# Kernel tuning notes

Measured on AMD Instinct MI355X. Metric: run time of the kernel, lower is better.

Reference implementation:

```python
import jax, jax.numpy as jnp
import numpy as np

SEQ, BATCH, IN_F, STATE, OUT_F = 2048, 32, 256, 512, 256


def setup_inputs() -> dict:
    key = jax.random.key(0)
    k1, k2, k3, k4 = jax.random.split(key, 4)
    x = jax.random.normal(k1, (SEQ, BATCH, IN_F), dtype=jnp.float32)
    # lambda_log init per module __init__ with rmin=0, rmax=1:
    # u ~ U(0,1); lambda_log = log(-0.5*log(u*(rmax+rmin)*(rmax-rmin)+rmin^2)) = log(-0.5*log(u))
    u = jax.random.uniform(k2, (STATE,), dtype=jnp.float32, minval=1e-6, maxval=1.0)
    lambda_log = jnp.log(-0.5 * jnp.log(u))
    B = jax.random.normal(k3, (STATE, IN_F), dtype=jnp.float32) / np.float32(np.sqrt(IN_F))
    C = jax.random.normal(k4, (OUT_F, STATE), dtype=jnp.float32) / np.float32(np.sqrt(STATE))
    return {"input": x, "lambda_log": lambda_log, "B": B, "C": C}


def reference(input, lambda_log, B, C):
    # mode='sequential', inner_loops=1, rnn_burnin=0, done=None, hidden=None
    lamda = jnp.exp(-jnp.exp(lambda_log))                 # [N]
    gamma = jnp.sqrt(1.0 - lamda * lamda + 1e-7)          # [N]
    # project all timesteps at once: b_seq[s,b,n] = gamma_n * (x_s @ B^T)
    b_seq = jnp.einsum('sbi,ni->sbn', input, B) * gamma   # [S,B,N]

    def step(state, b_t):
        new_state = lamda * state + b_t                   # diagonal LRU recurrence
        return new_state, new_state

    init = jnp.zeros((input.shape[1], lambda_log.shape[0]), dtype=input.dtype)
    final_state, states = jax.lax.scan(step, init, b_seq)  # states: [S,B,N]
    output = jnp.einsum('sbn,on->sbo', states, C)          # [S,B,O]
    return output, final_state
```

## Files before the change

### kernel.cpp

```cpp
#include <hip/hip_runtime.h>

#define SEQ   2048
#define BATCH 32
#define INF   256
#define NST   512
#define OUTF  256
#define CLEN  32
#define NCH   64
#define NJOB  4
#define NCG   (NCH / NJOB)
#define NBLK  (NCG * BATCH)

typedef __bf16 bf16;
typedef __bf16 bf16x8 __attribute__((ext_vector_type(8)));
typedef float  f32x4  __attribute__((ext_vector_type(4)));
typedef unsigned long long ull;

__global__ void k_prep(const float* __restrict__ ll,
                       const float* __restrict__ Bm,
                       const float* __restrict__ Cm,
                       float* __restrict__ lam,
                       float* __restrict__ lamG,
                       float* __restrict__ l2la,
                       bf16* __restrict__ Bb,
                       bf16* __restrict__ Cb) {
  int i = blockIdx.x * 256 + threadIdx.x;
  if (i < NST) {
    float e = expf(ll[i]);
    float lmb = expf(-e);
    lam[i] = lmb;
    l2la[i] = -e * 1.44269504088896341f;
    float p = lmb;
#pragma unroll
    for (int q = 0; q < 7; ++q) p *= p;
    lamG[i] = p;
  }
  if (i < NST * INF) {
    int n = i >> 8;
    float lmb = expf(-expf(ll[n]));
    float g = sqrtf(1.0f - lmb * lmb + 1e-7f);
    Bb[i] = (bf16)(Bm[i] * g);
  }
  if (i < OUTF * NST) {
    Cb[i] = (bf16)(Cm[i]);
  }
}

__device__ __forceinline__ void xload(const float* __restrict__ xp, int tid,
                                      float4 xr[4]) {
#pragma unroll
  for (int rep = 0; rep < 4; ++rep) {
    int slot = rep * 512 + tid;
    int row = slot >> 6, col4 = slot & 63;
    xr[rep] = *(const float4*)(xp + (size_t)row * (BATCH * INF) + col4 * 4);
  }
}

__device__ __forceinline__ void xstore(char* xsb, int tid, const float4 xr[4]) {
#pragma unroll
  for (int rep = 0; rep < 4; ++rep) {
    int slot = rep * 512 + tid;
    int row = slot >> 6, col4 = slot & 63;
    union { bf16 h[4]; ull u; } pk;
    pk.h[0] = (bf16)xr[rep].x; pk.h[1] = (bf16)xr[rep].y;
    pk.h[2] = (bf16)xr[rep].z; pk.h[3] = (bf16)xr[rep].w;
    int byte = (row * (INF * 2) + col4 * 8) ^ ((row & 15) << 4);
    *(ull*)(xsb + byte) = pk.u;
  }
}

__device__ __forceinline__ void reg_scan(f32x4 acc[2][4], float carry[4],
                                         const float la[4], const float l4[4],
                                         int kg, int rl) {
#pragma unroll
  for (int mt = 0; mt < 2; ++mt) {
    float sl[4][4];
#pragma unroll
    for (int nt = 0; nt < 4; ++nt) {
      sl[nt][0] = acc[mt][nt][0];
      sl[nt][1] = fmaf(la[nt], sl[nt][0], acc[mt][nt][1]);
      sl[nt][2] = fmaf(la[nt], sl[nt][1], acc[mt][nt][2]);
      sl[nt][3] = fmaf(la[nt], sl[nt][2], acc[mt][nt][3]);
    }
    float G[4];
#pragma unroll
    for (int nt = 0; nt < 4; ++nt) {
      float g1 = __shfl_up(sl[nt][3], 16);
      G[nt] = (kg >= 1) ? fmaf(l4[nt], g1, sl[nt][3]) : sl[nt][3];
    }
#pragma unroll
    for (int nt = 0; nt < 4; ++nt) {
      float l8 = l4[nt] * l4[nt];
      float g2 = __shfl_up(G[nt], 32);
      G[nt] = (kg >= 2) ? fmaf(l8, g2, G[nt]) : G[nt];
    }
#pragma unroll
    for (int nt = 0; nt < 4; ++nt) {
      float X = __shfl_up(G[nt], 16);
      X = (kg >= 1) ? X : 0.0f;
      float l8 = l4[nt] * l4[nt];
      float p4k = ((kg & 1) ? l4[nt] : 1.0f) * ((kg & 2) ? l8 : 1.0f);
      float cin = fmaf(p4k, carry[nt], X);
      float l2 = la[nt] * la[nt], l3 = l2 * la[nt];
      acc[mt][nt][0] = fmaf(la[nt], cin, sl[nt][0]);
      acc[mt][nt][1] = fmaf(l2, cin, sl[nt][1]);
      acc[mt][nt][2] = fmaf(l3, cin, sl[nt][2]);
      acc[mt][nt][3] = fmaf(l4[nt], cin, sl[nt][3]);
    }
#pragma unroll
    for (int nt = 0; nt < 4; ++nt)
      carry[nt] = __shfl(acc[mt][nt][3], rl + 48);
  }
}

__device__ __forceinline__ void gemm1_l2(const char* xsb, const bf16* __restrict__ Bb,
                                         f32x4 acc[2][4], int n0, int rl, int kg) {
#pragma unroll
  for (int k = 0; k < 8; ++k) {
    bf16x8 af[2], bfr[4];
#pragma unroll
    for (int mt = 0; mt < 2; ++mt) {
      int row = mt * 16 + rl;
      int byte = (row * (INF * 2) + (k * 32 + kg * 8) * 2) ^ (rl << 4);
      af[mt] = *(const bf16x8*)(xsb + byte);
    }
#pragma unroll
    for (int nt = 0; nt < 4; ++nt)
      bfr[nt] = *(const bf16x8*)(Bb + (size_t)(n0 + nt * 16 + rl) * INF + k * 32 + kg * 8);
#pragma unroll
    for (int mt = 0; mt < 2; ++mt)
#pragma unroll
      for (int nt = 0; nt < 4; ++nt)
        acc[mt][nt] = __builtin_amdgcn_mfma_f32_16x16x32_bf16(af[mt], bfr[nt], acc[mt][nt], 0, 0, 0);
  }
}

__global__ __launch_bounds__(512, 2)
void k_pass0f(const float* __restrict__ x, const bf16* __restrict__ Bb,
              const float* __restrict__ lam, float* __restrict__ Z,
              ull* __restrict__ bfrag) {
  __shared__ __align__(16) char xs[2][CLEN * INF * 2];

  const int tid = threadIdx.x, wid = tid >> 6, lane = tid & 63;
  const int rl = lane & 15, kg = lane >> 4;
  const int b = blockIdx.x >> 4, cg = blockIdx.x & 15;
  const int n0 = wid * 64;

  float la[4], l4[4], carry[4];
#pragma unroll
  for (int nt = 0; nt < 4; ++nt) {
    float v = lam[n0 + nt * 16 + rl];
    la[nt] = v; l4[nt] = (v * v) * (v * v);
    carry[nt] = 0.0f;
  }

  bf16x8 Breg[8][4];
#pragma unroll
  for (int k = 0; k < 8; ++k)
#pragma unroll
    for (int nt = 0; nt < 4; ++nt)
      Breg[k][nt] = *(const bf16x8*)(Bb + (size_t)(n0 + nt * 16 + rl) * INF + k * 32 + kg * 8);

  {
    float4 xr0[4];
    xload(x + ((size_t)(cg * NJOB * CLEN) * BATCH + b) * INF, tid, xr0);
    xstore(xs[0], tid, xr0);
  }
  __syncthreads();

#pragma unroll
  for (int jj = 0; jj < NJOB; ++jj) {
    const int c = cg * NJOB + jj;
    f32x4 acc[2][4] = {};
#pragma unroll
    for (int k = 0; k < 8; ++k) {
      bf16x8 af[2];
#pragma unroll
      for (int mt = 0; mt < 2; ++mt) {
        int row = mt * 16 + rl;
        int byte = (row * (INF * 2) + (k * 32 + kg * 8) * 2) ^ (rl << 4);
        af[mt] = *(const bf16x8*)(&xs[jj & 1][0] + byte);
      }
#pragma unroll
      for (int mt = 0; mt < 2; ++mt)
#pragma unroll
        for (int nt = 0; nt < 4; ++nt)
          acc[mt][nt] = __builtin_amdgcn_mfma_f32_16x16x32_bf16(af[mt], Breg[k][nt], acc[mt][nt], 0, 0, 0);
    }

    float4 xr[4];
    if (jj < NJOB - 1)
      xload(x + ((size_t)((c + 1) * CLEN) * BATCH + b) * INF, tid, xr);

    reg_scan(acc, carry, la, l4, kg, rl);

    {
      ull* dst = bfrag + ((size_t)(((cg * BATCH + b) * NJOB + jj) * 8 + wid)) * 512 + lane;
#pragma unroll
      for (int mt = 0; mt < 2; ++mt)
#pragma unroll
        for (int nt = 0; nt < 4; ++nt) {
          union { bf16 h[4]; ull u; } pk;
          pk.h[0] = (bf16)acc[mt][nt][0];
          pk.h[1] = (bf16)acc[mt][nt][1];
          pk.h[2] = (bf16)acc[mt][nt][2];
          pk.h[3] = (bf16)acc[mt][nt][3];
          dst[(mt * 4 + nt) * 64] = pk.u;
        }
    }

    if (jj < NJOB - 1) {
      xstore(xs[(jj + 1) & 1], tid, xr);
      __syncthreads();
    } else {
      if (kg == 0)
#pragma unroll
        for (int nt = 0; nt < 4; ++nt)
          Z[((size_t)cg * BATCH + b) * NST + n0 + nt * 16 + rl] = carry[nt];
    }
  }
}

__global__ __launch_bounds__(128)
void k_chain(const float* __restrict__ Z, const float* __restrict__ lamG,
             float* __restrict__ S0, float* __restrict__ fin) {
  const int b = blockIdx.x;
  const int n = blockIdx.y * 128 + threadIdx.x;
  const float lG = lamG[n];
  float z[NCG];
#pragma unroll
  for (int g = 0; g < NCG; ++g)
    z[g] = Z[((size_t)g * BATCH + b) * NST + n];
  float s = 0.0f;
#pragma unroll
  for (int g = 0; g < NCG; ++g) {
    S0[((size_t)g * BATCH + b) * NST + n] = s;
    s = fmaf(lG, s, z[g]);
  }
  fin[(size_t)b * NST + n] = s;
}

__global__ __launch_bounds__(512)
void k_gemm2c(const ull* __restrict__ bfrag, const bf16* __restrict__ Cb,
              const float* __restrict__ S0, const float* __restrict__ l2la,
              float* __restrict__ out) {
  __shared__ __align__(16) char ss[64 * NST * 2];

  const int tid = threadIdx.x, wid = tid >> 6, lane = tid & 63;
  const int rl = lane & 15, kg = lane >> 4;
  const int c2 = blockIdx.x >> 5, b = blockIdx.x & 31;
  const int cg = c2 >> 1;

  const ull* src8 = bfrag +
      ((size_t)((cg * BATCH + b) * NJOB + (c2 & 1) * 2)) * 4096;
  const float* S0g = S0 + ((size_t)cg * BATCH + b) * NST;
#pragma unroll
  for (int q = 0; q < 16; ++q) {
    int chunk = q * 512 + tid;
    int jjh = chunk >> 12;
    int within = chunk & 4095;
    int widx = within >> 9;
    int fr = (within >> 6) & 7;
    int mt = fr >> 2, nt = fr & 3;
    int ls = within & 63;
    int kgs = ls >> 4, rls = ls & 15;
    int n = widx * 64 + nt * 16 + rls;
    int t0 = jjh * 32 + mt * 16 + kgs * 4;
    int dt0 = (c2 & 1) * 64 + t0;

    union { ull u; bf16 h[4]; } in;
    in.u = src8[chunk];
    float l2 = l2la[n];
    float s0 = S0g[n];
    float e = exp2f((float)(dt0 + 1) * l2);
    float lm = exp2f(l2);
#pragma unroll
    for (int r = 0; r < 4; ++r) {
      float s = fmaf(e, s0, (float)in.h[r]);
      int t = t0 + r;
      int byte = (t * (NST * 2) + n * 2) ^ ((t & 15) << 4);
      *(bf16*)(&ss[0] + byte) = (bf16)s;
      e *= lm;
    }
  }
  __syncthreads();

  const int o0 = wid * 32;
  f32x4 acc[4][2] = {};
#pragma unroll
  for (int kq = 0; kq < 16; ++kq) {
    const int k0 = kq * 32;
    bf16x8 af[4], cf[2];
#pragma unroll
    for (int mf = 0; mf < 4; ++mf) {
      int t = mf * 16 + rl;
      af[mf] = *(const bf16x8*)(&ss[0] +
          ((t * (NST * 2) + (k0 + kg * 8) * 2) ^ ((t & 15) << 4)));
    }
#pragma unroll
    for (int ot2 = 0; ot2 < 2; ++ot2)
      cf[ot2] = *(const bf16x8*)(Cb + (size_t)(o0 + ot2 * 16 + rl) * NST + k0 + kg * 8);
#pragma unroll
    for (int mf = 0; mf < 4; ++mf)
#pragma unroll
      for (int ot2 = 0; ot2 < 2; ++ot2)
        acc[mf][ot2] = __builtin_amdgcn_mfma_f32_16x16x32_bf16(af[mf], cf[ot2], acc[mf][ot2], 0, 0, 0);
  }

#pragma unroll
  for (int mf = 0; mf < 4; ++mf)
#pragma unroll
    for (int ot2 = 0; ot2 < 2; ++ot2)
#pragma unroll
      for (int r = 0; r < 4; ++r) {
        int ml = mf * 16 + kg * 4 + r;
        size_t srow = (size_t)c2 * 64 + ml;
        int o = o0 + ot2 * 16 + rl;
        out[(srow * BATCH + b) * OUTF + o] = acc[mf][ot2][r];
      }
}

__global__ __launch_bounds__(512, 2)
void k_pass0_fb(const float* __restrict__ x, const bf16* __restrict__ Bb,
                const float* __restrict__ lam, float* __restrict__ Z) {
  __shared__ __align__(16) char xs[2][CLEN * INF * 2];

  const int tid = threadIdx.x, wid = tid >> 6, lane = tid & 63;
  const int rl = lane & 15, kg = lane >> 4;
  const int b = blockIdx.x >> 4, cg = blockIdx.x & 15;
  const int n0 = wid * 64;

  float la[4], l4[4], carry[4];
#pragma unroll
  for (int nt = 0; nt < 4; ++nt) {
    float v = lam[n0 + nt * 16 + rl];
    la[nt] = v; l4[nt] = (v * v) * (v * v);
    carry[nt] = 0.0f;
  }

  bf16x8 Breg[8][4];
#pragma unroll
  for (int k = 0; k < 8; ++k)
#pragma unroll
    for (int nt = 0; nt < 4; ++nt)
      Breg[k][nt] = *(const bf16x8*)(Bb + (size_t)(n0 + nt * 16 + rl) * INF + k * 32 + kg * 8);

  {
    float4 xr0[4];
    xload(x + ((size_t)(cg * NJOB * CLEN) * BATCH + b) * INF, tid, xr0);
    xstore(xs[0], tid, xr0);
  }
  __syncthreads();

#pragma unroll
  for (int jj = 0; jj < NJOB; ++jj) {
    const int c = cg * NJOB + jj;
    f32x4 acc[2][4] = {};
#pragma unroll
    for (int k = 0; k < 8; ++k) {
      bf16x8 af[2];
#pragma unroll
      for (int mt = 0; mt < 2; ++mt) {
        int row = mt * 16 + rl;
        int byte = (row * (INF * 2) + (k * 32 + kg * 8) * 2) ^ (rl << 4);
        af[mt] = *(const bf16x8*)(&xs[jj & 1][0] + byte);
      }
#pragma unroll
      for (int mt = 0; mt < 2; ++mt)
#pragma unroll
        for (int nt = 0; nt < 4; ++nt)
          acc[mt][nt] = __builtin_amdgcn_mfma_f32_16x16x32_bf16(af[mt], Breg[k][nt], acc[mt][nt], 0, 0, 0);
    }

    if (jj < NJOB - 1) {
      float4 xr[4];
      xload(x + ((size_t)((c + 1) * CLEN) * BATCH + b) * INF, tid, xr);
      reg_scan(acc, carry, la, l4, kg, rl);
      xstore(xs[(jj + 1) & 1], tid, xr);
      __syncthreads();
    } else {
      reg_scan(acc, carry, la, l4, kg, rl);
      if (kg == 0)
#pragma unroll
        for (int nt = 0; nt < 4; ++nt)
          Z[((size_t)cg * BATCH + b) * NST + n0 + nt * 16 + rl] = carry[nt];
    }
  }
}

__global__ __launch_bounds__(512)
void k_pass1_fb(const float* __restrict__ x, const bf16* __restrict__ Bb,
                const bf16* __restrict__ Cb, const float* __restrict__ lam,
                const float* __restrict__ S0, float* __restrict__ out,
                float* __restrict__ fin) {
  __shared__ __align__(16) char xs[2][CLEN * INF * 2];
  __shared__ __align__(16) char ss[CLEN * NST * 2];

  const int tid = threadIdx.x, wid = tid >> 6, lane = tid & 63;
  const int rl = lane & 15, kg = lane >> 4;
  const int b = blockIdx.x >> 4, cg = blockIdx.x & 15;
  const int n0 = wid * 64;

  float la[4], l4[4], carry[4];
#pragma unroll
  for (int nt = 0; nt < 4; ++nt) {
    float v = lam[n0 + nt * 16 + rl];
    la[nt] = v; l4[nt] = (v * v) * (v * v);
    carry[nt] = S0[((size_t)cg * BATCH + b) * NST + n0 + nt * 16 + rl];
  }
  {
    float4 xr0[4];
    xload(x + ((size_t)(cg * NJOB * CLEN) * BATCH + b) * INF, tid, xr0);
    xstore(xs[0], tid, xr0);
  }
  __syncthreads();

#pragma unroll
  for (int jj = 0; jj < NJOB; ++jj) {
    const int c = cg * NJOB + jj;
    f32x4 acc[2][4] = {};
    gemm1_l2(&xs[jj & 1][0], Bb, acc, n0, rl, kg);
    {
      float4 xr[4];
      const int lastj = (jj == NJOB - 1);
      if (!lastj)
        xload(x + ((size_t)((c + 1) * CLEN) * BATCH + b) * INF, tid, xr);
      reg_scan(acc, carry, la, l4, kg, rl);
      if (c == NCH - 1 && kg == 0)
#pragma unroll
        for (int nt = 0; nt < 4; ++nt)
          fin[(size_t)b * NST + n0 + nt * 16 + rl] = carry[nt];
      __syncthreads();
#pragma unroll
      for (int mt = 0; mt < 2; ++mt)
#pragma unroll
        for (int nt = 0; nt < 4; ++nt)
#pragma unroll
          for (int r = 0; r < 4; ++r) {
            int t = mt * 16 + kg * 4 + r;
            int n = n0 + nt * 16 + rl;
            int byte = (t * (NST * 2) + n * 2) ^ ((t & 15) << 4);
            *(bf16*)(&ss[0] + byte) = (bf16)acc[mt][nt][r];
          }
      if (!lastj) xstore(xs[(jj + 1) & 1], tid, xr);
    }
    __syncthreads();

    const int o0 = wid * 32;
    f32x4 a2[2][2] = {};
#pragma unroll
    for (int k0 = 0; k0 < NST; k0 += 32) {
      bf16x8 af[2], cf[2];
#pragma unroll
      for (int mt = 0; mt < 2; ++mt) {
        int t = mt * 16 + rl;
        int byte = (t * (NST * 2) + (k0 + kg * 8) * 2) ^ (rl << 4);
        af[mt] = *(const bf16x8*)(&ss[0] + byte);
      }
#pragma unroll
      for (int ot = 0; ot < 2; ++ot)
        cf[ot] = *(const bf16x8*)(Cb + (size_t)(o0 + ot * 16 + rl) * NST + k0 + kg * 8);
#pragma unroll
      for (int mt = 0; mt < 2; ++mt)
#pragma unroll
        for (int ot = 0; ot < 2; ++ot)
          a2[mt][ot] = __builtin_amdgcn_mfma_f32_16x16x32_bf16(af[mt], cf[ot], a2[mt][ot], 0, 0, 0);
    }
#pragma unroll
    for (int mt = 0; mt < 2; ++mt)
#pragma unroll
      for (int ot = 0; ot < 2; ++ot)
#pragma unroll
        for (int r = 0; r < 4; ++r) {
          int t = mt * 16 + kg * 4 + r;
          int o = o0 + ot * 16 + rl;
          out[(((size_t)(c * CLEN + t)) * BATCH + b) * OUTF + o] = a2[mt][ot][r];
        }
  }
}

extern "C" void kernel_launch(void* const* d_in, const int* in_sizes, int n_in,
                              void* d_out, int out_size, void* d_ws, size_t ws_size,
                              hipStream_t stream) {
  const float* x  = (const float*)d_in[0];
  const float* ll = (const float*)d_in[1];
  const float* Bm = (const float*)d_in[2];
  const float* Cm = (const float*)d_in[3];

  char* ws = (char*)d_ws;
  float* lam  = (float*)(ws);
  float* lamG = (float*)(ws + 2048);
  float* l2la = (float*)(ws + 4096);
  bf16*  Bb   = (bf16*)(ws + 6144);
  bf16*  Cb   = (bf16*)(ws + 6144 + NST * INF * 2);
  float* Z    = (float*)(ws + 6144 + NST * INF * 2 + OUTF * NST * 2);
  float* S0   = (float*)((char*)Z + (size_t)NCG * BATCH * NST * 4);
  ull*   bfrag= (ull*)((char*)S0 + (size_t)NCG * BATCH * NST * 4);
  const size_t NEED = ((char*)bfrag - ws) + (size_t)SEQ * BATCH * NST * 2;

  float* out = (float*)d_out;
  float* fin = out + (size_t)SEQ * BATCH * OUTF;

  k_prep<<<dim3(512), dim3(256), 0, stream>>>(ll, Bm, Cm, lam, lamG, l2la, Bb, Cb);
  if (ws_size >= NEED) {
    k_pass0f<<<dim3(NBLK), dim3(512), 0, stream>>>(x, Bb, lam, Z, bfrag);
    k_chain<<<dim3(BATCH, 4), dim3(128), 0, stream>>>(Z, lamG, S0, fin);
    k_gemm2c<<<dim3(1024), dim3(512), 0, stream>>>(bfrag, Cb, S0, l2la, out);
  } else {
    k_pass0_fb<<<dim3(NBLK), dim3(512), 0, stream>>>(x, Bb, lam, Z);
    k_chain<<<dim3(BATCH, 4), dim3(128), 0, stream>>>(Z, lamG, S0, fin);
    k_pass1_fb<<<dim3(NBLK), dim3(512), 0, stream>>>(x, Bb, Cb, lam, S0, out, fin);
  }
}
```

Before: 98.66 us.

## Deepen x prefetch in pass0 and halve gemm2 tile with C register prefetch

In k_pass0f, x is now prefetched two chunks ahead into four LDS buffers instead of double-buffered one ahead. The sync moves to just after the scan, so the global load has more time to overlap the MFMA and scan work. The output GEMM kernel now processes 32 timesteps per block instead of 64, launching 2048 blocks with half the LDS each to raise occupancy and parallelism. It also software-pipelines the C fragment loads across k iterations. Halving the tile cuts reuse of each C fragment and doubles C traffic, and quadrupling the pass0 LDS buffer may limit occupancy.

```diff
diff --git a/kernel.cpp b/kernel.cpp
--- a/kernel.cpp
+++ b/kernel.cpp
@@ -139,7 +139,7 @@
 void k_pass0f(const float* __restrict__ x, const bf16* __restrict__ Bb,
               const float* __restrict__ lam, float* __restrict__ Z,
               ull* __restrict__ bfrag) {
-  __shared__ __align__(16) char xs[2][CLEN * INF * 2];
+  __shared__ __align__(16) char xs[4][CLEN * INF * 2];
 
   const int tid = threadIdx.x, wid = tid >> 6, lane = tid & 63;
   const int rl = lane & 15, kg = lane >> 4;
@@ -162,9 +162,11 @@
       Breg[k][nt] = *(const bf16x8*)(Bb + (size_t)(n0 + nt * 16 + rl) * INF + k * 32 + kg * 8);
 
   {
-    float4 xr0[4];
-    xload(x + ((size_t)(cg * NJOB * CLEN) * BATCH + b) * INF, tid, xr0);
-    xstore(xs[0], tid, xr0);
+    float4 xr[4];
+    xload(x + ((size_t)(cg * NJOB * CLEN) * BATCH + b) * INF, tid, xr);
+    xstore(xs[0], tid, xr);
+    xload(x + ((size_t)((cg * NJOB + 1) * CLEN) * BATCH + b) * INF, tid, xr);
+    xstore(xs[1], tid, xr);
   }
   __syncthreads();
 
@@ -179,7 +181,7 @@
       for (int mt = 0; mt < 2; ++mt) {
         int row = mt * 16 + rl;
         int byte = (row * (INF * 2) + (k * 32 + kg * 8) * 2) ^ (rl << 4);
-        af[mt] = *(const bf16x8*)(&xs[jj & 1][0] + byte);
+        af[mt] = *(const bf16x8*)(&xs[jj][0] + byte);
       }
 #pragma unroll
       for (int mt = 0; mt < 2; ++mt)
@@ -189,10 +191,15 @@
     }
 
     float4 xr[4];
-    if (jj < NJOB - 1)
-      xload(x + ((size_t)((c + 1) * CLEN) * BATCH + b) * INF, tid, xr);
+    if (jj < 2)
+      xload(x + ((size_t)((c + 2) * CLEN) * BATCH + b) * INF, tid, xr);
 
     reg_scan(acc, carry, la, l4, kg, rl);
+
+    if (jj < 2) {
+      xstore(xs[jj + 2], tid, xr);
+      __syncthreads();
+    }
 
     {
       ull* dst = bfrag + ((size_t)(((cg * BATCH + b) * NJOB + jj) * 8 + wid)) * 512 + lane;
@@ -209,10 +216,7 @@
         }
     }
 
-    if (jj < NJOB - 1) {
-      xstore(xs[(jj + 1) & 1], tid, xr);
-      __syncthreads();
-    } else {
+    if (jj == NJOB - 1) {
       if (kg == 0)
 #pragma unroll
         for (int nt = 0; nt < 4; ++nt)
@@ -241,32 +245,29 @@
 }
 
 __global__ __launch_bounds__(512)
-void k_gemm2c(const ull* __restrict__ bfrag, const bf16* __restrict__ Cb,
+void k_gemm2d(const ull* __restrict__ bfrag, const bf16* __restrict__ Cb,
               const float* __restrict__ S0, const float* __restrict__ l2la,
               float* __restrict__ out) {
-  __shared__ __align__(16) char ss[64 * NST * 2];
+  __shared__ __align__(16) char ss[32 * NST * 2];
 
   const int tid = threadIdx.x, wid = tid >> 6, lane = tid & 63;
   const int rl = lane & 15, kg = lane >> 4;
-  const int c2 = blockIdx.x >> 5, b = blockIdx.x & 31;
-  const int cg = c2 >> 1;
-
-  const ull* src8 = bfrag +
-      ((size_t)((cg * BATCH + b) * NJOB + (c2 & 1) * 2)) * 4096;
+  const int c = blockIdx.x >> 5, b = blockIdx.x & 31;
+  const int cg = c >> 2, jj = c & 3;
+
+  const ull* src8 = bfrag + ((size_t)((cg * BATCH + b) * NJOB + jj)) * 4096;
   const float* S0g = S0 + ((size_t)cg * BATCH + b) * NST;
 #pragma unroll
-  for (int q = 0; q < 16; ++q) {
+  for (int q = 0; q < 8; ++q) {
     int chunk = q * 512 + tid;
-    int jjh = chunk >> 12;
-    int within = chunk & 4095;
-    int widx = within >> 9;
-    int fr = (within >> 6) & 7;
+    int widx = chunk >> 9;
+    int fr = (chunk >> 6) & 7;
     int mt = fr >> 2, nt = fr & 3;
-    int ls = within & 63;
+    int ls = chunk & 63;
     int kgs = ls >> 4, rls = ls & 15;
     int n = widx * 64 + nt * 16 + rls;
-    int t0 = jjh * 32 + mt * 16 + kgs * 4;
-    int dt0 = (c2 & 1) * 64 + t0;
+    int t0 = mt * 16 + kgs * 4;
+    int dt0 = jj * 32 + t0;
 
     union { ull u; bf16 h[4]; } in;
     in.u = src8[chunk];
@@ -286,35 +287,44 @@
   __syncthreads();
 
   const int o0 = wid * 32;
-  f32x4 acc[4][2] = {};
+  f32x4 acc[2][2] = {};
+  bf16x8 cf[2];
+#pragma unroll
+  for (int ot2 = 0; ot2 < 2; ++ot2)
+    cf[ot2] = *(const bf16x8*)(Cb + (size_t)(o0 + ot2 * 16 + rl) * NST + kg * 8);
 #pragma unroll
   for (int kq = 0; kq < 16; ++kq) {
     const int k0 = kq * 32;
-    bf16x8 af[4], cf[2];
-#pragma unroll
-    for (int mf = 0; mf < 4; ++mf) {
+    bf16x8 cfn[2];
+    if (kq < 15)
+#pragma unroll
+      for (int ot2 = 0; ot2 < 2; ++ot2)
+        cfn[ot2] = *(const bf16x8*)(Cb + (size_t)(o0 + ot2 * 16 + rl) * NST + k0 + 32 + kg * 8);
+    bf16x8 af[2];
+#pragma unroll
+    for (int mf = 0; mf < 2; ++mf) {
       int t = mf * 16 + rl;
       af[mf] = *(const bf16x8*)(&ss[0] +
           ((t * (NST * 2) + (k0 + kg * 8) * 2) ^ ((t & 15) << 4)));
     }
 #pragma unroll
-    for (int ot2 = 0; ot2 < 2; ++ot2)
-      cf[ot2] = *(const bf16x8*)(Cb + (size_t)(o0 + ot2 * 16 + rl) * NST + k0 + kg * 8);
-#pragma unroll
-    for (int mf = 0; mf < 4; ++mf)
+    for (int mf = 0; mf < 2; ++mf)
 #pragma unroll
       for (int ot2 = 0; ot2 < 2; ++ot2)
         acc[mf][ot2] = __builtin_amdgcn_mfma_f32_16x16x32_bf16(af[mf], cf[ot2], acc[mf][ot2], 0, 0, 0);
-  }
-
-#pragma unroll
-  for (int mf = 0; mf < 4; ++mf)
+    if (kq < 15) {
+      cf[0] = cfn[0]; cf[1] = cfn[1];
+    }
+  }
+
+#pragma unroll
+  for (int mf = 0; mf < 2; ++mf)
 #pragma unroll
     for (int ot2 = 0; ot2 < 2; ++ot2)
 #pragma unroll
       for (int r = 0; r < 4; ++r) {
         int ml = mf * 16 + kg * 4 + r;
-        size_t srow = (size_t)c2 * 64 + ml;
+        size_t srow = (size_t)c * 32 + ml;
         int o = o0 + ot2 * 16 + rl;
         out[(srow * BATCH + b) * OUTF + o] = acc[mf][ot2][r];
       }
@@ -505,7 +515,7 @@
   if (ws_size >= NEED) {
     k_pass0f<<<dim3(NBLK), dim3(512), 0, stream>>>(x, Bb, lam, Z, bfrag);
     k_chain<<<dim3(BATCH, 4), dim3(128), 0, stream>>>(Z, lamG, S0, fin);
-    k_gemm2c<<<dim3(1024), dim3(512), 0, stream>>>(bfrag, Cb, S0, l2la, out);
+    k_gemm2d<<<dim3(2048), dim3(512), 0, stream>>>(bfrag, Cb, S0, l2la, out);
   } else {
     k_pass0_fb<<<dim3(NBLK), dim3(512), 0, stream>>>(x, Bb, lam, Z);
     k_chain<<<dim3(BATCH, 4), dim3(128), 0, stream>>>(Z, lamG, S0, fin);
```

New measurement: 121.2 us. 22.9% more time.
